# Kernel optimization log

Measured on AMD Instinct MI355X. Metric: run time of the kernel, lower is better.

## Reference

```python
import jax, jax.numpy as jnp
import numpy as np

B, DIN, DH, DOUT, E, GIN, GH = 16384, 480, 512, 360, 8, 64, 128


def setup_inputs() -> dict:
    key = jax.random.key(0)
    ks = jax.random.split(key, 16)

    def glorot(k, shape):
        bound = np.sqrt(6.0 / np.prod(shape[-2:]))
        return jax.random.uniform(k, shape, jnp.float32, -bound, bound)

    return {
        "x": jax.random.normal(ks[0], (B, DIN), jnp.float32),
        # norm stats: row0 = mean, row1 = std (kept away from 0)
        "Xnorm": jnp.stack([jax.random.normal(ks[1], (DIN,)) * 0.1,
                            jax.random.uniform(ks[2], (DIN,), minval=0.5, maxval=1.5)]),
        "Ynorm": jnp.stack([jax.random.normal(ks[3], (DOUT,)) * 0.1,
                            jax.random.uniform(ks[4], (DOUT,), minval=0.5, maxval=1.5)]),
        "G1_W": glorot(ks[5], (GIN, GH)), "G1_b": jnp.zeros((GH,), jnp.float32),
        "G2_W": glorot(ks[6], (GH, GH)), "G2_b": jnp.zeros((GH,), jnp.float32),
        "G3_W": glorot(ks[7], (GH, E)),  "G3_b": jnp.zeros((E,), jnp.float32),
        "W1": glorot(ks[8], (E, DIN, DH)), "b1": jnp.zeros((E, DH), jnp.float32),
        "W2": glorot(ks[9], (E, DH, DH)),  "b2": jnp.zeros((E, DH), jnp.float32),
        "W3": glorot(ks[10], (E, DH, DOUT)), "b3": jnp.zeros((E, DOUT), jnp.float32),
        "gating_indices": jnp.arange(GIN, dtype=jnp.int32),
    }


def expert_linear(h, w, W, b):
    # h: [B, I], w: [B, E], W: [E, I, O], b: [E, O]
    # sum_e w[:,e] * (h @ W[e] + b[e])
    y = jnp.einsum('bi,eio->beo', h, W)        # [B, E, O]
    return jnp.einsum('be,beo->bo', w, y) + w @ b


def reference(x, Xnorm, Ynorm, G1_W, G1_b, G2_W, G2_b, G3_W, G3_b,
              W1, b1, W2, b2, W3, b3, gating_indices):
    xn = (x - Xnorm[0]) / Xnorm[1]
    # gating network (dropout inactive at eval)
    g = xn[:, gating_indices]
    g = jax.nn.elu(g @ G1_W + G1_b)
    g = jax.nn.elu(g @ G2_W + G2_b)
    w = jax.nn.softmax(g @ G3_W + G3_b, axis=1)   # [B, E]
    # expert-blended main network
    m = jax.nn.elu(expert_linear(xn, w, W1, b1))
    m = jax.nn.elu(expert_linear(m, w, W2, b2))
    m = expert_linear(m, w, W3, b3)
    return m * Ynorm[1] + Ynorm[0]
```

## Files before the change

### kernel.cpp

```cpp
#include <hip/hip_runtime.h>
#include <hip/hip_bf16.h>
#include <math.h>

#define BATCH 16384
#define DIN   480
#define DH    512
#define DOUT  360
#define NEXP  8
#define GIN   64
#define GH    128
#define KP    512

typedef short bf16x8 __attribute__((ext_vector_type(8)));
typedef float f32x4  __attribute__((ext_vector_type(4)));

__device__ __forceinline__ short f2bf(float f) {
    __hip_bfloat16 h = __float2bfloat16(f);
    return *reinterpret_cast<short*>(&h);
}
__device__ __forceinline__ float eluf(float x) { return x > 0.f ? x : expf(x) - 1.f; }

__device__ __forceinline__ void gll16(const void* g, void* l) {
    __builtin_amdgcn_global_load_lds(
        (const __attribute__((address_space(1))) unsigned int*)g,
        (__attribute__((address_space(3))) unsigned int*)l, 16, 0, 0);
}

__global__ void prep_xn_kernel(const float* __restrict__ x,
                               const float* __restrict__ Xnorm,
                               short* __restrict__ xnbf) {
    const int tid = blockIdx.x * 256 + threadIdx.x;
    const int row = tid >> 6;
    const int c   = (tid & 63) * 8;
    short v8[8];
    if (c < DIN) {
        #pragma unroll
        for (int j = 0; j < 8; ++j) {
            float v = (x[(size_t)row * DIN + c + j] - Xnorm[c + j]) / Xnorm[DIN + c + j];
            v8[j] = f2bf(v);
        }
    } else {
        #pragma unroll
        for (int j = 0; j < 8; ++j) v8[j] = 0;
    }
    *(uint4*)&xnbf[(size_t)row * KP + c] = *(uint4*)v8;
}

__global__ void transpose_w_kernel(const float* __restrict__ src,
                                   short* __restrict__ dst,
                                   int K, int N, int NPAD) {
    __shared__ float tile[32][33];
    const int ntn = NPAD / 32;
    const int ntk = KP / 32;
    int lin = blockIdx.x;
    const int e  = lin / (ntk * ntn);
    lin -= e * ntk * ntn;
    const int kt = lin / ntn;
    const int nt = lin % ntn;
    const int t = threadIdx.x;
    #pragma unroll
    for (int r = 0; r < 4; ++r) {
        int idx = t + r * 256;
        int i = idx >> 5;
        int j = idx & 31;
        int k = kt * 32 + i;
        int n = nt * 32 + j;
        float v = (n < N && k < K) ? src[((size_t)e * K + k) * N + n] : 0.f;
        tile[i][j] = v;
    }
    __syncthreads();
    #pragma unroll
    for (int r = 0; r < 4; ++r) {
        int idx = t + r * 256;
        int i2 = idx & 31;
        int j2 = idx >> 5;
        dst[((size_t)e * NPAD + nt * 32 + j2) * KP + kt * 32 + i2] = f2bf(tile[i2][j2]);
    }
}

__global__ __launch_bounds__(256) void gating_kernel(
    const float* __restrict__ x, const float* __restrict__ Xnorm,
    const float* __restrict__ G1W, const float* __restrict__ G1b,
    const float* __restrict__ G2W, const float* __restrict__ G2b,
    const float* __restrict__ G3W, const float* __restrict__ G3b,
    const int* __restrict__ gidx, float* __restrict__ wout) {

    __shared__ float g2s[GH * GH];
    __shared__ float g3s[GH * NEXP];
    __shared__ float b1s[GH], b2s[GH], b3s[NEXP];
    __shared__ float g0b[4][GIN], h1b[4][GH], h2b[4][GH];

    const int t = threadIdx.x;
    const int lane = t & 63;
    const int wid  = t >> 6;

    for (int i = t; i < GH * GH; i += 256) g2s[i] = G2W[i];
    for (int i = t; i < GH * NEXP; i += 256) g3s[i] = G3W[i];
    if (t < GH) { b1s[t] = G1b[t]; b2s[t] = G2b[t]; }
    if (t < NEXP) b3s[t] = G3b[t];
    __syncthreads();

    const int gi = gidx[lane];
    const float mu = Xnorm[gi];
    const float inv_sig = 1.f / Xnorm[DIN + gi];

    for (int it = 0; it < 16; ++it) {
        const int row = (blockIdx.x * 4 + wid) * 16 + it;
        float g0 = (x[(size_t)row * DIN + gi] - mu) * inv_sig;
        g0b[wid][lane] = g0;
        __syncthreads();
        float h1a = b1s[lane], h1c = b1s[lane + 64];
        #pragma unroll 8
        for (int i = 0; i < GIN; ++i) {
            float g = g0b[wid][i];
            h1a += g * G1W[i * GH + lane];
            h1c += g * G1W[i * GH + lane + 64];
        }
        h1b[wid][lane] = eluf(h1a);
        h1b[wid][lane + 64] = eluf(h1c);
        __syncthreads();
        float h2a = b2s[lane], h2c = b2s[lane + 64];
        #pragma unroll 8
        for (int i = 0; i < GH; ++i) {
            float h = h1b[wid][i];
            h2a += h * g2s[i * GH + lane];
            h2c += h * g2s[i * GH + lane + 64];
        }
        h2b[wid][lane] = eluf(h2a);
        h2b[wid][lane + 64] = eluf(h2c);
        __syncthreads();
        const int e  = lane & 7;
        const int ch = lane >> 3;
        float p = 0.f;
        #pragma unroll
        for (int i2 = 0; i2 < 16; ++i2) {
            int i = ch * 16 + i2;
            p += h2b[wid][i] * g3s[i * NEXP + e];
        }
        p += __shfl_xor(p, 8);
        p += __shfl_xor(p, 16);
        p += __shfl_xor(p, 32);
        p += b3s[e];
        float mx = p;
        mx = fmaxf(mx, __shfl_xor(mx, 1));
        mx = fmaxf(mx, __shfl_xor(mx, 2));
        mx = fmaxf(mx, __shfl_xor(mx, 4));
        float ex = expf(p - mx);
        float sm = ex;
        sm += __shfl_xor(sm, 1);
        sm += __shfl_xor(sm, 2);
        sm += __shfl_xor(sm, 4);
        float wv = ex / sm;
        if (lane < NEXP) wout[(size_t)row * NEXP + lane] = wv;
        __syncthreads();
    }
}

template<int NPAD, int NREAL, int MODE>
__global__ __launch_bounds__(512, 2) void expert_v8_kernel(
    const short* __restrict__ A, const short* __restrict__ Wt,
    const float* __restrict__ wgate, const float* __restrict__ bias,
    const float* __restrict__ Ynorm, void* __restrict__ Out) {

    __shared__ __align__(16) short bufA[2][256 * 64];
    __shared__ __align__(16) short bufB[3][128 * 64];
    __shared__ float wlsT[NEXP][256];

    const int t = threadIdx.x;
    const int lane = t & 63;
    const int wid  = t >> 6;
    const int wr = wid >> 1;
    const int wc = wid & 1;
    const int l4 = lane >> 4, lr = lane & 15;

    constexpr int NN = NPAD / 128;
    constexpr int nwg = (BATCH / 256) * NN;
    constexpr int cpx = nwg / 8;
    const int lb  = (blockIdx.x & 7) * cpx + (blockIdx.x >> 3);
    const int m0  = (lb / NN) * 256;
    const int n0  = (lb % NN) * 128;

    for (int i = t; i < NEXP * 256; i += 512) {
        int e = i >> 8, r = i & 255;
        wlsT[e][r] = wgate[(size_t)(m0 + r) * NEXP + e];
    }

    const int srow  = lane >> 3;
    const int sslot = (lane & 7) ^ srow;

    const short* baseA[4];
    #pragma unroll
    for (int i = 0; i < 4; ++i)
        baseA[i] = A + (size_t)(m0 + (wid * 4 + i) * 8 + srow) * KP + sslot * 8;
    const short* baseB[2];
    #pragma unroll
    for (int i = 0; i < 2; ++i)
        baseB[i] = Wt + (size_t)(n0 + (wid * 2 + i) * 8 + srow) * KP + sslot * 8;

    short* const bufA0 = &bufA[0][0];
    short* const bufB0 = &bufB[0][0];

    f32x4 accF[4][4];
    #pragma unroll
    for (int mi = 0; mi < 4; ++mi)
        #pragma unroll
        for (int ni = 0; ni < 4; ++ni)
            accF[mi][ni] = (f32x4){0.f, 0.f, 0.f, 0.f};
    const f32x4 zf = (f32x4){0.f, 0.f, 0.f, 0.f};

    #pragma unroll
    for (int i = 0; i < 4; ++i)
        gll16(baseA[i], bufA0 + (wid * 4 + i) * 512);
    #pragma unroll
    for (int i = 0; i < 2; ++i)
        gll16(baseB[i], bufB0 + (wid * 2 + i) * 512);
    #pragma unroll
    for (int i = 0; i < 2; ++i)
        gll16(baseB[i] + (size_t)NPAD * KP, bufB0 + 128 * 64 + (wid * 2 + i) * 512);
    __syncthreads();

    const int xo0 = (l4 * 8) ^ ((lr & 7) << 3);
    const int xo1 = (32 + l4 * 8) ^ ((lr & 7) << 3);
    const int arow = (wr * 64 + lr) * 64;
    const int brow = (wc * 64 + lr) * 64;

    int kB = 0;
    #pragma unroll 1
    for (int kt = 0; kt < 8; ++kt) {
        const short* Ab = bufA0 + (kt & 1) * (256 * 64);

        bf16x8 af0[4], af1[4];
        #pragma unroll
        for (int mi = 0; mi < 4; ++mi) {
            af0[mi] = *(const bf16x8*)(Ab + arow + mi * 1024 + xo0);
            af1[mi] = *(const bf16x8*)(Ab + arow + mi * 1024 + xo1);
        }

        #pragma unroll 1
        for (int e = 0; e < 8; ++e) {
            const short* Bb = bufB0 + kB * (128 * 64);
            const int kB2 = (kB >= 1) ? kB - 1 : kB + 2;

            if (kt < 7 || e < 6) {
                const int e2  = (e + 2) & 7;
                const int kt2 = kt + ((e + 2) >> 3);
                const size_t ob = (size_t)e2 * NPAD * KP + (size_t)kt2 * 64;
                #pragma unroll
                for (int i = 0; i < 2; ++i)
                    gll16(baseB[i] + ob, bufB0 + kB2 * (128 * 64) + (wid * 2 + i) * 512);
            }
            if (e == 6 && kt < 7) {
                const size_t oa = (size_t)(kt + 1) * 64;
                #pragma unroll
                for (int i = 0; i < 4; ++i)
                    gll16(baseA[i] + oa,
                          bufA0 + ((kt + 1) & 1) * (256 * 64) + (wid * 4 + i) * 512);
            }

            f32x4 acc[4][4];

            {
                bf16x8 b0[4];
                #pragma unroll
                for (int ni = 0; ni < 4; ++ni)
                    b0[ni] = *(const bf16x8*)(Bb + brow + ni * 1024 + xo0);
                __builtin_amdgcn_s_setprio(1);
                #pragma unroll
                for (int mi = 0; mi < 4; ++mi)
                    #pragma unroll
                    for (int ni = 0; ni < 4; ++ni)
                        acc[mi][ni] = __builtin_amdgcn_mfma_f32_16x16x32_bf16(
                            af0[mi], b0[ni], zf, 0, 0, 0);
                __builtin_amdgcn_s_setprio(0);
            }
            {
                bf16x8 b1[4];
                #pragma unroll
                for (int ni = 0; ni < 4; ++ni)
                    b1[ni] = *(const bf16x8*)(Bb + brow + ni * 1024 + xo1);
                __builtin_amdgcn_s_setprio(1);
                #pragma unroll
                for (int mi = 0; mi < 4; ++mi)
                    #pragma unroll
                    for (int ni = 0; ni < 4; ++ni)
                        acc[mi][ni] = __builtin_amdgcn_mfma_f32_16x16x32_bf16(
                            af1[mi], b1[ni], acc[mi][ni], 0, 0, 0);
                __builtin_amdgcn_s_setprio(0);
            }

            {
                f32x4 wv[4];
                #pragma unroll
                for (int mi = 0; mi < 4; ++mi)
                    wv[mi] = *(const f32x4*)&wlsT[e][wr * 64 + mi * 16 + l4 * 4];
                #pragma unroll
                for (int mi = 0; mi < 4; ++mi)
                    #pragma unroll
                    for (int ni = 0; ni < 4; ++ni)
                        #pragma unroll
                        for (int j = 0; j < 4; ++j)
                            accF[mi][ni][j] += wv[mi][j] * acc[mi][ni][j];
            }

            if (kt == 7 && e >= 6)      asm volatile("s_waitcnt vmcnt(0)" ::: "memory");
            else if (e == 6)            asm volatile("s_waitcnt vmcnt(6)" ::: "memory");
            else                        asm volatile("s_waitcnt vmcnt(2)" ::: "memory");
            asm volatile("s_barrier" ::: "memory");

            kB = (kB == 2) ? 0 : kB + 1;
        }
    }

    {
        float bv[4][NEXP];
        #pragma unroll
        for (int ni = 0; ni < 4; ++ni) {
            int ng = n0 + wc * 64 + ni * 16 + lr;
            #pragma unroll
            for (int e = 0; e < NEXP; ++e)
                bv[ni][e] = (ng < NREAL) ? bias[(size_t)e * NREAL + ng] : 0.f;
        }
        #pragma unroll
        for (int mi = 0; mi < 4; ++mi) {
            f32x4 wve[NEXP];
            #pragma unroll
            for (int e = 0; e < NEXP; ++e)
                wve[e] = *(const f32x4*)&wlsT[e][wr * 64 + mi * 16 + l4 * 4];
            #pragma unroll
            for (int ni = 0; ni < 4; ++ni)
                #pragma unroll
                for (int j = 0; j < 4; ++j) {
                    float sum = 0.f;
                    #pragma unroll
                    for (int e = 0; e < NEXP; ++e) sum += wve[e][j] * bv[ni][e];
                    accF[mi][ni][j] += sum;
                }
        }
    }

    #pragma unroll
    for (int mi = 0; mi < 4; ++mi) {
        #pragma unroll
        for (int j = 0; j < 4; ++j) {
            size_t rg = (size_t)(m0 + wr * 64 + mi * 16 + l4 * 4 + j);
            #pragma unroll
            for (int ni = 0; ni < 4; ++ni) {
                int ng = n0 + wc * 64 + ni * 16 + lr;
                float v = accF[mi][ni][j];
                if (MODE == 0) {
                    v = v > 0.f ? v : expf(v) - 1.f;
                    ((short*)Out)[rg * NPAD + ng] = f2bf(v);
                } else {
                    if (ng < NREAL)
                        ((float*)Out)[rg * NREAL + ng] = v * Ynorm[NREAL + ng] + Ynorm[ng];
                }
            }
        }
    }
}

extern "C" void kernel_launch(void* const* d_in, const int* in_sizes, int n_in,
                              void* d_out, int out_size, void* d_ws, size_t ws_size,
                              hipStream_t stream) {
    const float* x     = (const float*)d_in[0];
    const float* Xnorm = (const float*)d_in[1];
    const float* Ynorm = (const float*)d_in[2];
    const float* G1W   = (const float*)d_in[3];
    const float* G1b   = (const float*)d_in[4];
    const float* G2W   = (const float*)d_in[5];
    const float* G2b   = (const float*)d_in[6];
    const float* G3W   = (const float*)d_in[7];
    const float* G3b   = (const float*)d_in[8];
    const float* W1    = (const float*)d_in[9];
    const float* b1    = (const float*)d_in[10];
    const float* W2    = (const float*)d_in[11];
    const float* b2    = (const float*)d_in[12];
    const float* W3    = (const float*)d_in[13];
    const float* b3    = (const float*)d_in[14];
    const int*   gidx  = (const int*)d_in[15];

    char* ws = (char*)d_ws;
    size_t off = 0;
    short* xnbf = (short*)(ws + off); off += (size_t)BATCH * KP * 2;
    short* m1   = (short*)(ws + off); off += (size_t)BATCH * DH * 2;
    short* Wt1  = (short*)(ws + off); off += (size_t)NEXP * DH  * KP * 2;
    short* Wt2  = (short*)(ws + off); off += (size_t)NEXP * DH  * KP * 2;
    short* Wt3  = (short*)(ws + off); off += (size_t)NEXP * 384 * KP * 2;
    float* wg   = (float*)(ws + off); off += (size_t)BATCH * NEXP * 4;
    short* m2   = xnbf;
    if (off > ws_size) return;

    prep_xn_kernel<<<BATCH * 64 / 256, 256, 0, stream>>>(x, Xnorm, xnbf);

    transpose_w_kernel<<<NEXP * (KP / 32) * (DH / 32), 256, 0, stream>>>(W1, Wt1, DIN, DH, DH);
    transpose_w_kernel<<<NEXP * (KP / 32) * (DH / 32), 256, 0, stream>>>(W2, Wt2, DH, DH, DH);
    transpose_w_kernel<<<NEXP * (KP / 32) * (384 / 32), 256, 0, stream>>>(W3, Wt3, DH, DOUT, 384);

    gating_kernel<<<256, 256, 0, stream>>>(x, Xnorm, G1W, G1b, G2W, G2b, G3W, G3b, gidx, wg);

    expert_v8_kernel<DH, DH, 0>
        <<<(BATCH / 256) * (DH / 128), 512, 0, stream>>>(xnbf, Wt1, wg, b1, Ynorm, m1);
    expert_v8_kernel<DH, DH, 0>
        <<<(BATCH / 256) * (DH / 128), 512, 0, stream>>>(m1, Wt2, wg, b2, Ynorm, m2);
    expert_v8_kernel<384, DOUT, 1>
        <<<(BATCH / 256) * (384 / 128), 512, 0, stream>>>(m2, Wt3, wg, b3, Ynorm, (void*)d_out);
}
```

Measured before the change: 326.0 us.

## Prefetch next expert's first B fragment into registers across steps

The expert loop is unrolled by two with ping-pong register buffers, so each step's first-half B fragments come from LDS during the previous step. This is meant to hide LDS read latency before the first MFMA block. The wait before each barrier becomes a full vmcnt(0) instead of the graded counts, which can stall on in-flight global-to-LDS loads and adds register pressure under launch bounds of 2 blocks.

```diff
diff --git a/kernel.cpp b/kernel.cpp
--- a/kernel.cpp
+++ b/kernel.cpp
@@ -156,8 +156,71 @@
     }
 }
 
+#define EXPERT_STEP(EVAL, BCU, BCF)                                            \
+{                                                                              \
+    const int e_ = (EVAL);                                                     \
+    const int s_ = kt * 8 + e_;                                                \
+    const short* Bb = bufB0 + kB * (128 * 64);                                 \
+    const int kB1 = (kB == 2) ? 0 : kB + 1;                                    \
+    const int kB2 = (kB1 == 2) ? 0 : kB1 + 1;                                  \
+    if (s_ < 62) {                                                             \
+        const int s2 = s_ + 2;                                                 \
+        const size_t ob = (size_t)(s2 & 7) * NPAD * KP + (size_t)(s2 >> 3) * 64; \
+        _Pragma("unroll")                                                      \
+        for (int i = 0; i < 2; ++i)                                            \
+            gll16(baseB[i] + ob, bufB0 + kB2 * (128 * 64) + (wid * 2 + i) * 512); \
+    }                                                                          \
+    if (e_ == 6 && kt < 7) {                                                   \
+        const size_t oa = (size_t)(kt + 1) * 64;                               \
+        _Pragma("unroll")                                                      \
+        for (int i = 0; i < 4; ++i)                                            \
+            gll16(baseA[i] + oa, bufA0 + ((kt + 1) & 1) * (256 * 64) + (wid * 4 + i) * 512); \
+    }                                                                          \
+    if (s_ < 63) {                                                             \
+        const short* Bn = bufB0 + kB1 * (128 * 64);                            \
+        _Pragma("unroll")                                                      \
+        for (int ni = 0; ni < 4; ++ni)                                         \
+            BCF[ni] = *(const bf16x8*)(Bn + brow + ni * 1024 + xo0);           \
+    }                                                                          \
+    f32x4 wv[4];                                                               \
+    _Pragma("unroll")                                                          \
+    for (int mi = 0; mi < 4; ++mi)                                             \
+        wv[mi] = *(const f32x4*)&wlsT[e_][wr * 64 + mi * 16 + l4 * 4];         \
+    f32x4 acc[4][4];                                                           \
+    __builtin_amdgcn_s_setprio(1);                                             \
+    _Pragma("unroll")                                                          \
+    for (int mi = 0; mi < 4; ++mi)                                             \
+        _Pragma("unroll")                                                      \
+        for (int ni = 0; ni < 4; ++ni)                                         \
+            acc[mi][ni] = __builtin_amdgcn_mfma_f32_16x16x32_bf16(             \
+                af0[mi], BCU[ni], zf, 0, 0, 0);                                \
+    __builtin_amdgcn_s_setprio(0);                                             \
+    bf16x8 b1[4];                                                              \
+    _Pragma("unroll")                                                          \
+    for (int ni = 0; ni < 4; ++ni)                                             \
+        b1[ni] = *(const bf16x8*)(Bb + brow + ni * 1024 + xo1);                \
+    __builtin_amdgcn_s_setprio(1);                                             \
+    _Pragma("unroll")                                                          \
+    for (int mi = 0; mi < 4; ++mi)                                             \
+        _Pragma("unroll")                                                      \
+        for (int ni = 0; ni < 4; ++ni)                                         \
+            acc[mi][ni] = __builtin_amdgcn_mfma_f32_16x16x32_bf16(             \
+                af1[mi], b1[ni], acc[mi][ni], 0, 0, 0);                        \
+    __builtin_amdgcn_s_setprio(0);                                             \
+    _Pragma("unroll")                                                          \
+    for (int mi = 0; mi < 4; ++mi)                                             \
+        _Pragma("unroll")                                                      \
+        for (int ni = 0; ni < 4; ++ni)                                         \
+            _Pragma("unroll")                                                  \
+            for (int j = 0; j < 4; ++j)                                        \
+                accF[mi][ni][j] += wv[mi][j] * acc[mi][ni][j];                 \
+    asm volatile("s_waitcnt vmcnt(0)" ::: "memory");                           \
+    asm volatile("s_barrier" ::: "memory");                                    \
+    kB = kB1;                                                                  \
+}
+
 template<int NPAD, int NREAL, int MODE>
-__global__ __launch_bounds__(512, 2) void expert_v8_kernel(
+__global__ __launch_bounds__(512, 2) void expert_v9_kernel(
     const short* __restrict__ A, const short* __restrict__ Wt,
     const float* __restrict__ wgate, const float* __restrict__ bias,
     const float* __restrict__ Ynorm, void* __restrict__ Out) {
@@ -224,6 +287,11 @@
     const int arow = (wr * 64 + lr) * 64;
     const int brow = (wc * 64 + lr) * 64;
 
+    bf16x8 bcA[4], bcB[4];
+    #pragma unroll
+    for (int ni = 0; ni < 4; ++ni)
+        bcA[ni] = *(const bf16x8*)(bufB0 + brow + ni * 1024 + xo0);
+
     int kB = 0;
     #pragma unroll 1
     for (int kt = 0; kt < 8; ++kt) {
@@ -237,77 +305,9 @@
         }
 
         #pragma unroll 1
-        for (int e = 0; e < 8; ++e) {
-            const short* Bb = bufB0 + kB * (128 * 64);
-            const int kB2 = (kB >= 1) ? kB - 1 : kB + 2;
-
-            if (kt < 7 || e < 6) {
-                const int e2  = (e + 2) & 7;
-                const int kt2 = kt + ((e + 2) >> 3);
-                const size_t ob = (size_t)e2 * NPAD * KP + (size_t)kt2 * 64;
-                #pragma unroll
-                for (int i = 0; i < 2; ++i)
-                    gll16(baseB[i] + ob, bufB0 + kB2 * (128 * 64) + (wid * 2 + i) * 512);
-            }
-            if (e == 6 && kt < 7) {
-                const size_t oa = (size_t)(kt + 1) * 64;
-                #pragma unroll
-                for (int i = 0; i < 4; ++i)
-                    gll16(baseA[i] + oa,
-                          bufA0 + ((kt + 1) & 1) * (256 * 64) + (wid * 4 + i) * 512);
-            }
-
-            f32x4 acc[4][4];
-
-            {
-                bf16x8 b0[4];
-                #pragma unroll
-                for (int ni = 0; ni < 4; ++ni)
-                    b0[ni] = *(const bf16x8*)(Bb + brow + ni * 1024 + xo0);
-                __builtin_amdgcn_s_setprio(1);
-                #pragma unroll
-                for (int mi = 0; mi < 4; ++mi)
-                    #pragma unroll
-                    for (int ni = 0; ni < 4; ++ni)
-                        acc[mi][ni] = __builtin_amdgcn_mfma_f32_16x16x32_bf16(
-                            af0[mi], b0[ni], zf, 0, 0, 0);
-                __builtin_amdgcn_s_setprio(0);
-            }
-            {
-                bf16x8 b1[4];
-                #pragma unroll
-                for (int ni = 0; ni < 4; ++ni)
-                    b1[ni] = *(const bf16x8*)(Bb + brow + ni * 1024 + xo1);
-                __builtin_amdgcn_s_setprio(1);
-                #pragma unroll
-                for (int mi = 0; mi < 4; ++mi)
-                    #pragma unroll
-                    for (int ni = 0; ni < 4; ++ni)
-                        acc[mi][ni] = __builtin_amdgcn_mfma_f32_16x16x32_bf16(
-                            af1[mi], b1[ni], acc[mi][ni], 0, 0, 0);
-                __builtin_amdgcn_s_setprio(0);
-            }
-
-            {
-                f32x4 wv[4];
-                #pragma unroll
-                for (int mi = 0; mi < 4; ++mi)
-                    wv[mi] = *(const f32x4*)&wlsT[e][wr * 64 + mi * 16 + l4 * 4];
-                #pragma unroll
-                for (int mi = 0; mi < 4; ++mi)
-                    #pragma unroll
-                    for (int ni = 0; ni < 4; ++ni)
-                        #pragma unroll
-                        for (int j = 0; j < 4; ++j)
-                            accF[mi][ni][j] += wv[mi][j] * acc[mi][ni][j];
-            }
-
-            if (kt == 7 && e >= 6)      asm volatile("s_waitcnt vmcnt(0)" ::: "memory");
-            else if (e == 6)            asm volatile("s_waitcnt vmcnt(6)" ::: "memory");
-            else                        asm volatile("s_waitcnt vmcnt(2)" ::: "memory");
-            asm volatile("s_barrier" ::: "memory");
-
-            kB = (kB == 2) ? 0 : kB + 1;
+        for (int ee = 0; ee < 4; ++ee) {
+            EXPERT_STEP(2 * ee,     bcA, bcB)
+            EXPERT_STEP(2 * ee + 1, bcB, bcA)
         }
     }
 
@@ -398,10 +398,10 @@
 
     gating_kernel<<<256, 256, 0, stream>>>(x, Xnorm, G1W, G1b, G2W, G2b, G3W, G3b, gidx, wg);
 
-    expert_v8_kernel<DH, DH, 0>
+    expert_v9_kernel<DH, DH, 0>
         <<<(BATCH / 256) * (DH / 128), 512, 0, stream>>>(xnbf, Wt1, wg, b1, Ynorm, m1);
-    expert_v8_kernel<DH, DH, 0>
+    expert_v9_kernel<DH, DH, 0>
         <<<(BATCH / 256) * (DH / 128), 512, 0, stream>>>(m1, Wt2, wg, b2, Ynorm, m2);
-    expert_v8_kernel<384, DOUT, 1>
+    expert_v9_kernel<384, DOUT, 1>
         <<<(BATCH / 256) * (384 / 128), 512, 0, stream>>>(m2, Wt3, wg, b3, Ynorm, (void*)d_out);
 }
```

Result: slower. 530.0 us (+62.6%).
